# Optimization experiments

Hardware: AMD Instinct MI355X
Metric: run time of the kernel (lower is better)

The kernel has to match this reference:

```python
import jax, jax.numpy as jnp
import numpy as np

B = 262144
NUM_FEA = 256          # input feature dim, split into two towers of 128
HIDDEN = [64, 32, 16]  # tower hidden units
CO_FEA = 32            # 2 * HIDDEN[-1], features entering co-attention
EMB = 8                # per-feature embedding dim
OUT_DIM = 16           # final Dense(16)


def setup_inputs() -> dict:
    key = jax.random.key(0)
    ks = jax.random.split(key, 12)
    mid = NUM_FEA // 2
    def glorot(k, shape):
        fan_in, fan_out = shape[0], shape[1]
        lim = np.sqrt(6.0 / (fan_in + fan_out)).astype(np.float32)
        return jax.random.uniform(k, shape, jnp.float32, -lim, lim)
    return {
        "x": jax.random.normal(ks[0], (B, NUM_FEA), jnp.float32),
        # shared tower (weight_share=True -> only mod_dnn1 is used)
        "W1": glorot(ks[1], (mid, HIDDEN[0])), "b1": jnp.zeros((HIDDEN[0],), jnp.float32),
        "W2": glorot(ks[2], (HIDDEN[0], HIDDEN[1])), "b2": jnp.zeros((HIDDEN[1],), jnp.float32),
        "W3": glorot(ks[3], (HIDDEN[1], HIDDEN[2])), "b3": jnp.zeros((HIDDEN[2],), jnp.float32),
        # 32 per-feature Dense(8) layers on scalar inputs, stacked: weight [32,8], bias [32,8]
        "W_emb": glorot(ks[4], (CO_FEA, EMB)),
        "b_emb": jnp.zeros((CO_FEA, EMB), jnp.float32),
        # bilinear co-attention matrix
        "M": glorot(ks[5], (EMB, EMB)),
        # final Dense(16, relu) for mix='concat'
        "W_out": glorot(ks[6], (CO_FEA, OUT_DIM)),
        "b_out": jnp.zeros((OUT_DIM,), jnp.float32),
    }


def reference(x, W1, b1, W2, b2, W3, b3, W_emb, b_emb, M, W_out, b_out):
    mid = x.shape[1] // 2

    def tower(h):
        h = jax.nn.relu(h @ W1 + b1)
        h = jax.nn.relu(h @ W2 + b2)
        h = jax.nn.relu(h @ W3 + b3)
        return h

    left = tower(x[:, :mid])      # [B,16]
    right = tower(x[:, mid:])     # [B,16] (weight_share=True)
    out = jnp.concatenate([left, right], axis=-1)  # [B,32]

    # 32 tiny Dense(emb) on scalar features, batched: [B,32,1]*[32,8] + [32,8]
    emb = out[:, :, None] * W_emb[None, :, :] + b_emb[None, :, :]  # [B,32,8]
    cmid = out.shape[1] // 2  # 16
    l, r = emb[:, :cmid, :], emb[:, cmid:, :]

    G = jnp.tanh(jnp.einsum('bie,ef,bjf->bij', l, M, r))  # [B,16,16]
    lr = jax.nn.softmax(G.sum(axis=1), axis=-1)           # [B,16]
    rl = jax.nn.softmax(G.sum(axis=2), axis=-1)           # [B,16]
    a = jnp.concatenate([lr, rl], axis=-1)                # [B,32]

    out = out * a
    # mix == 'concat' -> Dense(16, relu)
    return jax.nn.relu(out @ W_out + b_out)               # [B,16]
```

## Files before the change

### kernel.cpp

```cpp
#include <hip/hip_runtime.h>

typedef __attribute__((ext_vector_type(8))) short bf16x8;
typedef __attribute__((ext_vector_type(4))) float f32x4;

#define MFMA16(a, b, c) __builtin_amdgcn_mfma_f32_16x16x32_bf16(a, b, c, 0, 0, 0)

__device__ __forceinline__ unsigned short f2bf(float f) {
    unsigned u = __builtin_bit_cast(unsigned, f);
    u += 0x7FFFu + ((u >> 16) & 1u);
    return (unsigned short)(u >> 16);
}
__device__ __forceinline__ float bf2f(unsigned short h) {
    return __builtin_bit_cast(float, (unsigned)h << 16);
}
__device__ __forceinline__ void split8(const float* v, bf16x8& hi, bf16x8& lo) {
    #pragma unroll
    for (int i = 0; i < 8; ++i) {
        unsigned short h = f2bf(v[i]);
        hi[i] = (short)h;
        lo[i] = (short)f2bf(v[i] - bf2f(h));
    }
}

__device__ __forceinline__ float fast_tanh(float x) {
    float e = __expf(2.0f * x);
    float r = __builtin_amdgcn_rcpf(e + 1.0f);
    return fmaf(-2.0f, r, 1.0f);
}

__global__ void prep_kernel(const float* __restrict__ W1,
                            const float* __restrict__ W2,
                            const float* __restrict__ W3,
                            const float* __restrict__ W_emb,
                            const float* __restrict__ b_emb,
                            const float* __restrict__ M,
                            float* __restrict__ pqrs,
                            unsigned short* __restrict__ w1h,
                            unsigned short* __restrict__ w1l,
                            unsigned short* __restrict__ wsm) {
    const int t = threadIdx.x;
    {
        const int j = t >> 4;
        const int i = t & 15;
        float mr[8], mb[8];
        #pragma unroll
        for (int e = 0; e < 8; ++e) {
            float ar = 0.f, ab = 0.f;
            #pragma unroll
            for (int f = 0; f < 8; ++f) {
                const float m = M[e * 8 + f];
                ar = fmaf(m, W_emb[(16 + j) * 8 + f], ar);
                ab = fmaf(m, b_emb[(16 + j) * 8 + f], ab);
            }
            mr[e] = ar; mb[e] = ab;
        }
        float P = 0.f, Q = 0.f, R = 0.f, S = 0.f;
        #pragma unroll
        for (int e = 0; e < 8; ++e) {
            const float lw = W_emb[i * 8 + e];
            const float lb = b_emb[i * 8 + e];
            P = fmaf(lw, mr[e], P);
            Q = fmaf(lw, mb[e], Q);
            R = fmaf(lb, mr[e], R);
            S = fmaf(lb, mb[e], S);
        }
        pqrs[0 * 256 + j * 16 + i] = P;
        pqrs[1 * 256 + j * 16 + i] = Q;
        pqrs[2 * 256 + j * 16 + i] = R;
        pqrs[3 * 256 + j * 16 + i] = S;
    }
    for (int e = 0; e < 32; ++e) {
        const int idx = t * 32 + e;
        const int i = idx & 7, lane = (idx >> 3) & 63;
        const int n = (idx >> 9) & 3, kt = idx >> 11;
        const int k = kt * 32 + (lane >> 4) * 8 + i;
        const int c = n * 16 + (lane & 15);
        const float v = W1[k * 64 + c];
        const unsigned short h = f2bf(v);
        w1h[idx] = h;
        w1l[idx] = f2bf(v - bf2f(h));
    }
    for (int e = 0; e < 8; ++e) {
        const int idx = t * 8 + e;
        const int i = idx & 7, lane = (idx >> 3) & 63;
        const int n = (idx >> 9) & 1, kt = (idx >> 10) & 1;
        const int k = kt * 32 + (lane >> 4) * 8 + i;
        const int c = n * 16 + (lane & 15);
        const float v = W2[k * 32 + c];
        const unsigned short h = f2bf(v);
        wsm[idx] = h;
        wsm[2048 + idx] = f2bf(v - bf2f(h));
    }
    for (int e = 0; e < 2; ++e) {
        const int idx = t * 2 + e;
        const int i = idx & 7, lane = (idx >> 3) & 63;
        const int k = (lane >> 4) * 8 + i;
        const int c = lane & 15;
        const float v = W3[k * 16 + c];
        const unsigned short h = f2bf(v);
        wsm[4096 + idx] = h;
        wsm[4608 + idx] = f2bf(v - bf2f(h));
    }
}

__global__ __launch_bounds__(256, 2) void fused_kernel(
    const float* __restrict__ x,
    const unsigned short* __restrict__ w1h,
    const unsigned short* __restrict__ w1l,
    const unsigned short* __restrict__ wsm,
    const float* __restrict__ b1, const float* __restrict__ b2,
    const float* __restrict__ b3,
    const float* __restrict__ pqrs,
    const float* __restrict__ W_out, const float* __restrict__ b_out,
    float* __restrict__ y) {
    __shared__ unsigned short s_wf[5120];
    __shared__ float s_tr[4][16 * 68];
    __shared__ float s_h3[4][64 * 20];

    const int tid = threadIdx.x;
    {
        const unsigned int* g = (const unsigned int*)wsm;
        unsigned int* s = (unsigned int*)s_wf;
        #pragma unroll
        for (int it = 0; it < 10; ++it) s[it * 256 + tid] = g[it * 256 + tid];
    }
    __syncthreads();

    const int l  = tid & 63;
    const int wv = tid >> 6;
    const int lm = l & 15;
    const int lg = l >> 4;

    const unsigned short* s_w2h = s_wf;
    const unsigned short* s_w2l = s_wf + 2048;
    const unsigned short* s_w3h = s_wf + 4096;
    const unsigned short* s_w3l = s_wf + 4608;

    float b1v[4], b2v[2];
    #pragma unroll
    for (int n = 0; n < 4; ++n) b1v[n] = b1[n * 16 + lm];
    #pragma unroll
    for (int n = 0; n < 2; ++n) b2v[n] = b2[n * 16 + lm];
    const float b3v = b3[lm];

    const long tr0 = (long)blockIdx.x * 256 + wv * 64;
    float* tb  = s_tr[wv];
    float* h3b = s_h3[wv];

    float4 xb[2][8];
    {
        const float* xp = x + (tr0 + lm) * 128 + lg * 8;
        #pragma unroll
        for (int kt = 0; kt < 4; ++kt) {
            xb[0][2 * kt]     = *(const float4*)(xp + kt * 32);
            xb[0][2 * kt + 1] = *(const float4*)(xp + kt * 32 + 4);
        }
    }

    #pragma unroll
    for (int tile = 0; tile < 4; ++tile) {
        const int cur = tile & 1, nxt = cur ^ 1;
        if (tile < 3) {
            const float* xp = x + (tr0 + (tile + 1) * 16 + lm) * 128 + lg * 8;
            #pragma unroll
            for (int kt = 0; kt < 4; ++kt) {
                xb[nxt][2 * kt]     = *(const float4*)(xp + kt * 32);
                xb[nxt][2 * kt + 1] = *(const float4*)(xp + kt * 32 + 4);
            }
        }
        f32x4 acc[4];
        #pragma unroll
        for (int n = 0; n < 4; ++n) acc[n] = f32x4{b1v[n], b1v[n], b1v[n], b1v[n]};
        #pragma unroll
        for (int kt = 0; kt < 4; ++kt) {
            const float4 a = xb[cur][2 * kt], b = xb[cur][2 * kt + 1];
            const float xv[8] = {a.x, a.y, a.z, a.w, b.x, b.y, b.z, b.w};
            bf16x8 xh, xl; split8(xv, xh, xl);
            #pragma unroll
            for (int n = 0; n < 4; ++n) {
                const int fo = ((kt * 4 + n) * 64 + l) * 8;
                const bf16x8 wh = *(const bf16x8*)(w1h + fo);
                const bf16x8 wl = *(const bf16x8*)(w1l + fo);
                acc[n] = MFMA16(xh, wh, acc[n]);
                acc[n] = MFMA16(xl, wh, acc[n]);
                acc[n] = MFMA16(xh, wl, acc[n]);
            }
        }
        #pragma unroll
        for (int n = 0; n < 4; ++n)
            #pragma unroll
            for (int r = 0; r < 4; ++r)
                tb[(lg * 4 + r) * 68 + n * 16 + lm] = fmaxf(acc[n][r], 0.f);
        f32x4 acc2[2];
        #pragma unroll
        for (int n = 0; n < 2; ++n) acc2[n] = f32x4{b2v[n], b2v[n], b2v[n], b2v[n]};
        #pragma unroll
        for (int kt = 0; kt < 2; ++kt) {
            const float* ap = tb + lm * 68 + kt * 32 + lg * 8;
            const float4 h0 = *(const float4*)(ap);
            const float4 h1 = *(const float4*)(ap + 4);
            const float hv[8] = {h0.x, h0.y, h0.z, h0.w, h1.x, h1.y, h1.z, h1.w};
            bf16x8 hh, hl; split8(hv, hh, hl);
            #pragma unroll
            for (int n = 0; n < 2; ++n) {
                const int fo = ((kt * 2 + n) * 64 + l) * 8;
                const bf16x8 wh = *(const bf16x8*)(s_w2h + fo);
                const bf16x8 wl = *(const bf16x8*)(s_w2l + fo);
                acc2[n] = MFMA16(hh, wh, acc2[n]);
                acc2[n] = MFMA16(hl, wh, acc2[n]);
                acc2[n] = MFMA16(hh, wl, acc2[n]);
            }
        }
        #pragma unroll
        for (int n = 0; n < 2; ++n)
            #pragma unroll
            for (int r = 0; r < 4; ++r)
                tb[(lg * 4 + r) * 68 + n * 16 + lm] = fmaxf(acc2[n][r], 0.f);
        f32x4 acc3 = f32x4{b3v, b3v, b3v, b3v};
        {
            const float* ap = tb + lm * 68 + lg * 8;
            const float4 h0 = *(const float4*)(ap);
            const float4 h1 = *(const float4*)(ap + 4);
            const float hv[8] = {h0.x, h0.y, h0.z, h0.w, h1.x, h1.y, h1.z, h1.w};
            bf16x8 hh, hl; split8(hv, hh, hl);
            const bf16x8 wh = *(const bf16x8*)(s_w3h + l * 8);
            const bf16x8 wl = *(const bf16x8*)(s_w3l + l * 8);
            acc3 = MFMA16(hh, wh, acc3);
            acc3 = MFMA16(hl, wh, acc3);
            acc3 = MFMA16(hh, wl, acc3);
        }
        #pragma unroll
        for (int r = 0; r < 4; ++r)
            h3b[(tile * 16 + lg * 4 + r) * 20 + lm] = fmaxf(acc3[r], 0.f);
    }

    const int p = l & 1;
    float o[16];
    {
        const float4* hp = (const float4*)(h3b + l * 20);
        const float4 t0 = hp[0], t1 = hp[1], t2 = hp[2], t3 = hp[3];
        o[0] = t0.x;  o[1] = t0.y;  o[2] = t0.z;  o[3] = t0.w;
        o[4] = t1.x;  o[5] = t1.y;  o[6] = t1.z;  o[7] = t1.w;
        o[8] = t2.x;  o[9] = t2.y;  o[10] = t2.z; o[11] = t2.w;
        o[12] = t3.x; o[13] = t3.y; o[14] = t3.z; o[15] = t3.w;
    }
    float oL[16], oR[16];
    #pragma unroll
    for (int i = 0; i < 16; ++i) {
        const float oth = __shfl_xor(o[i], 1);
        oL[i] = p ? oth : o[i];
        oR[i] = p ? o[i] : oth;
    }

    float si[16];
    #pragma unroll
    for (int i = 0; i < 16; ++i) si[i] = 0.f;
    float sj[16];
    #pragma unroll
    for (int j = 0; j < 16; ++j) {
        const float r = oR[j];
        const float* __restrict__ Pr = pqrs +       j * 16;
        const float* __restrict__ Qr = pqrs + 256 + j * 16;
        const float* __restrict__ Rr = pqrs + 512 + j * 16;
        const float* __restrict__ Sr = pqrs + 768 + j * 16;
        float accg = 0.f;
        #pragma unroll
        for (int i = 0; i < 16; ++i) {
            const float t1 = fmaf(r, Pr[i], Qr[i]);
            const float t2 = fmaf(r, Rr[i], Sr[i]);
            const float g  = fast_tanh(fmaf(oL[i], t1, t2));
            accg  += g;
            si[i] += g;
        }
        sj[j] = accg;
    }
    {
        float mx = sj[0];
        #pragma unroll
        for (int i = 1; i < 16; ++i) mx = fmaxf(mx, sj[i]);
        float s = 0.f; float ex[16];
        #pragma unroll
        for (int i = 0; i < 16; ++i) { ex[i] = __expf(sj[i] - mx); s += ex[i]; }
        const float inv = __builtin_amdgcn_rcpf(s);
        #pragma unroll
        for (int i = 0; i < 16; ++i) oL[i] *= ex[i] * inv;
    }
    {
        float mx = si[0];
        #pragma unroll
        for (int i = 1; i < 16; ++i) mx = fmaxf(mx, si[i]);
        float s = 0.f; float ex[16];
        #pragma unroll
        for (int i = 0; i < 16; ++i) { ex[i] = __expf(si[i] - mx); s += ex[i]; }
        const float inv = __builtin_amdgcn_rcpf(s);
        #pragma unroll
        for (int i = 0; i < 16; ++i) oR[i] *= ex[i] * inv;
    }

    float yv[16];
    #pragma unroll
    for (int oo = 0; oo < 16; ++oo) yv[oo] = b_out[oo];
    #pragma unroll
    for (int c = 0; c < 16; ++c) {
        const float cl = oL[c];
        const float cr = oR[c];
        const float* __restrict__ wl = W_out + c * 16;
        const float* __restrict__ wt = W_out + (16 + c) * 16;
        #pragma unroll
        for (int oo = 0; oo < 16; ++oo) {
            yv[oo] = fmaf(cl, wl[oo], yv[oo]);
            yv[oo] = fmaf(cr, wt[oo], yv[oo]);
        }
    }
    #pragma unroll
    for (int oo = 0; oo < 16; ++oo) yv[oo] = fmaxf(yv[oo], 0.f);

    float4 v0, v1;
    v0.x = p ? yv[8]  : yv[0]; v0.y = p ? yv[9]  : yv[1];
    v0.z = p ? yv[10] : yv[2]; v0.w = p ? yv[11] : yv[3];
    v1.x = p ? yv[12] : yv[4]; v1.y = p ? yv[13] : yv[5];
    v1.z = p ? yv[14] : yv[6]; v1.w = p ? yv[15] : yv[7];
    const long row = (tr0 >> 1) + (l >> 1);
    float* __restrict__ yo = y + row * 16 + p * 8;
    *reinterpret_cast<float4*>(yo)     = v0;
    *reinterpret_cast<float4*>(yo + 4) = v1;
}

extern "C" void kernel_launch(void* const* d_in, const int* in_sizes, int n_in,
                              void* d_out, int out_size, void* d_ws, size_t ws_size,
                              hipStream_t stream) {
    const float* x     = (const float*)d_in[0];
    const float* W1    = (const float*)d_in[1];
    const float* b1    = (const float*)d_in[2];
    const float* W2    = (const float*)d_in[3];
    const float* b2    = (const float*)d_in[4];
    const float* W3    = (const float*)d_in[5];
    const float* b3    = (const float*)d_in[6];
    const float* W_emb = (const float*)d_in[7];
    const float* b_emb = (const float*)d_in[8];
    const float* M     = (const float*)d_in[9];
    const float* W_out = (const float*)d_in[10];
    const float* b_out = (const float*)d_in[11];
    float* y = (float*)d_out;

    float* pqrs = (float*)d_ws;
    unsigned short* w1h = (unsigned short*)((char*)d_ws + 4096);
    unsigned short* w1l = w1h + 8192;
    unsigned short* wsm = w1l + 8192;

    const int nrows = in_sizes[0] / 256;

    prep_kernel<<<1, 256, 0, stream>>>(W1, W2, W3, W_emb, b_emb, M,
                                       pqrs, w1h, w1l, wsm);
    const int grid = nrows / 128;
    fused_kernel<<<grid, 256, 0, stream>>>(x, w1h, w1l, wsm,
                                           b1, b2, b3, pqrs, W_out, b_out, y);
}
```

Before: 152.4 us.

## Double rows per wave, drop LDS weight staging, fold tanh scaling

Each wave now processes 128 tower rows (64 output rows), so every lane owns one full output row and the shuffle-based left/right pairing goes away. W2/W3 fragments are read directly from global memory instead of being staged in LDS with a block barrier. The 2·log2(e) factor is folded into the precomputed P/Q/R/S so the inner loop uses exp2 plus rcp and applies the 1-2r affine once per row sum. The bf16 split uses packed v_cvt_pk_bf16_f32 and the launch bound asks for 3 blocks per CU. In exchange the grid is halved and global weight reads may add latency.

```diff
diff --git a/kernel.cpp b/kernel.cpp
--- a/kernel.cpp
+++ b/kernel.cpp
@@ -13,19 +13,23 @@
 __device__ __forceinline__ float bf2f(unsigned short h) {
     return __builtin_bit_cast(float, (unsigned)h << 16);
 }
+
 __device__ __forceinline__ void split8(const float* v, bf16x8& hi, bf16x8& lo) {
-    #pragma unroll
-    for (int i = 0; i < 8; ++i) {
-        unsigned short h = f2bf(v[i]);
-        hi[i] = (short)h;
-        lo[i] = (short)f2bf(v[i] - bf2f(h));
-    }
-}
-
-__device__ __forceinline__ float fast_tanh(float x) {
-    float e = __expf(2.0f * x);
-    float r = __builtin_amdgcn_rcpf(e + 1.0f);
-    return fmaf(-2.0f, r, 1.0f);
+    unsigned* hp = reinterpret_cast<unsigned*>(&hi);
+    unsigned* lp = reinterpret_cast<unsigned*>(&lo);
+    #pragma unroll
+    for (int q = 0; q < 4; ++q) {
+        const float a = v[2 * q], b = v[2 * q + 1];
+        unsigned hpair;
+        asm("v_cvt_pk_bf16_f32 %0, %1, %2" : "=v"(hpair) : "v"(a), "v"(b));
+        const float ha = __builtin_bit_cast(float, hpair << 16);
+        const float hb = __builtin_bit_cast(float, hpair & 0xFFFF0000u);
+        const float ra = a - ha, rb = b - hb;
+        unsigned lpair;
+        asm("v_cvt_pk_bf16_f32 %0, %1, %2" : "=v"(lpair) : "v"(ra), "v"(rb));
+        hp[q] = hpair;
+        lp[q] = lpair;
+    }
 }
 
 __global__ void prep_kernel(const float* __restrict__ W1,
@@ -39,6 +43,7 @@
                             unsigned short* __restrict__ w1l,
                             unsigned short* __restrict__ wsm) {
     const int t = threadIdx.x;
+    const float C2 = 2.8853900817779268f;
     {
         const int j = t >> 4;
         const int i = t & 15;
@@ -64,10 +69,10 @@
             R = fmaf(lb, mr[e], R);
             S = fmaf(lb, mb[e], S);
         }
-        pqrs[0 * 256 + j * 16 + i] = P;
-        pqrs[1 * 256 + j * 16 + i] = Q;
-        pqrs[2 * 256 + j * 16 + i] = R;
-        pqrs[3 * 256 + j * 16 + i] = S;
+        pqrs[0 * 256 + j * 16 + i] = C2 * P;
+        pqrs[1 * 256 + j * 16 + i] = C2 * Q;
+        pqrs[2 * 256 + j * 16 + i] = C2 * R;
+        pqrs[3 * 256 + j * 16 + i] = C2 * S;
     }
     for (int e = 0; e < 32; ++e) {
         const int idx = t * 32 + e;
@@ -103,7 +108,7 @@
     }
 }
 
-__global__ __launch_bounds__(256, 2) void fused_kernel(
+__global__ __launch_bounds__(256, 3) void fused_kernel(
     const float* __restrict__ x,
     const unsigned short* __restrict__ w1h,
     const unsigned short* __restrict__ w1l,
@@ -113,28 +118,19 @@
     const float* __restrict__ pqrs,
     const float* __restrict__ W_out, const float* __restrict__ b_out,
     float* __restrict__ y) {
-    __shared__ unsigned short s_wf[5120];
     __shared__ float s_tr[4][16 * 68];
-    __shared__ float s_h3[4][64 * 20];
+    __shared__ float s_h3[4][16 * 130];
 
     const int tid = threadIdx.x;
-    {
-        const unsigned int* g = (const unsigned int*)wsm;
-        unsigned int* s = (unsigned int*)s_wf;
-        #pragma unroll
-        for (int it = 0; it < 10; ++it) s[it * 256 + tid] = g[it * 256 + tid];
-    }
-    __syncthreads();
-
     const int l  = tid & 63;
     const int wv = tid >> 6;
     const int lm = l & 15;
     const int lg = l >> 4;
 
-    const unsigned short* s_w2h = s_wf;
-    const unsigned short* s_w2l = s_wf + 2048;
-    const unsigned short* s_w3h = s_wf + 4096;
-    const unsigned short* s_w3l = s_wf + 4608;
+    const unsigned short* w2h = wsm;
+    const unsigned short* w2l = wsm + 2048;
+    const unsigned short* w3h = wsm + 4096;
+    const unsigned short* w3l = wsm + 4608;
 
     float b1v[4], b2v[2];
     #pragma unroll
@@ -143,7 +139,7 @@
     for (int n = 0; n < 2; ++n) b2v[n] = b2[n * 16 + lm];
     const float b3v = b3[lm];
 
-    const long tr0 = (long)blockIdx.x * 256 + wv * 64;
+    const long tr0 = (long)blockIdx.x * 512 + wv * 128;
     float* tb  = s_tr[wv];
     float* h3b = s_h3[wv];
 
@@ -158,9 +154,9 @@
     }
 
     #pragma unroll
-    for (int tile = 0; tile < 4; ++tile) {
+    for (int tile = 0; tile < 8; ++tile) {
         const int cur = tile & 1, nxt = cur ^ 1;
-        if (tile < 3) {
+        if (tile < 7) {
             const float* xp = x + (tr0 + (tile + 1) * 16 + lm) * 128 + lg * 8;
             #pragma unroll
             for (int kt = 0; kt < 4; ++kt) {
@@ -204,8 +200,8 @@
             #pragma unroll
             for (int n = 0; n < 2; ++n) {
                 const int fo = ((kt * 2 + n) * 64 + l) * 8;
-                const bf16x8 wh = *(const bf16x8*)(s_w2h + fo);
-                const bf16x8 wl = *(const bf16x8*)(s_w2l + fo);
+                const bf16x8 wh = *(const bf16x8*)(w2h + fo);
+                const bf16x8 wl = *(const bf16x8*)(w2l + fo);
                 acc2[n] = MFMA16(hh, wh, acc2[n]);
                 acc2[n] = MFMA16(hl, wh, acc2[n]);
                 acc2[n] = MFMA16(hh, wl, acc2[n]);
@@ -223,39 +219,29 @@
             const float4 h1 = *(const float4*)(ap + 4);
             const float hv[8] = {h0.x, h0.y, h0.z, h0.w, h1.x, h1.y, h1.z, h1.w};
             bf16x8 hh, hl; split8(hv, hh, hl);
-            const bf16x8 wh = *(const bf16x8*)(s_w3h + l * 8);
-            const bf16x8 wl = *(const bf16x8*)(s_w3l + l * 8);
+            const bf16x8 wh = *(const bf16x8*)(w3h + l * 8);
+            const bf16x8 wl = *(const bf16x8*)(w3l + l * 8);
             acc3 = MFMA16(hh, wh, acc3);
             acc3 = MFMA16(hl, wh, acc3);
             acc3 = MFMA16(hh, wl, acc3);
         }
         #pragma unroll
         for (int r = 0; r < 4; ++r)
-            h3b[(tile * 16 + lg * 4 + r) * 20 + lm] = fmaxf(acc3[r], 0.f);
-    }
-
-    const int p = l & 1;
-    float o[16];
-    {
-        const float4* hp = (const float4*)(h3b + l * 20);
-        const float4 t0 = hp[0], t1 = hp[1], t2 = hp[2], t3 = hp[3];
-        o[0] = t0.x;  o[1] = t0.y;  o[2] = t0.z;  o[3] = t0.w;
-        o[4] = t1.x;  o[5] = t1.y;  o[6] = t1.z;  o[7] = t1.w;
-        o[8] = t2.x;  o[9] = t2.y;  o[10] = t2.z; o[11] = t2.w;
-        o[12] = t3.x; o[13] = t3.y; o[14] = t3.z; o[15] = t3.w;
-    }
+            h3b[lm * 130 + tile * 16 + lg * 4 + r] = fmaxf(acc3[r], 0.f);
+    }
+
     float oL[16], oR[16];
     #pragma unroll
-    for (int i = 0; i < 16; ++i) {
-        const float oth = __shfl_xor(o[i], 1);
-        oL[i] = p ? oth : o[i];
-        oR[i] = p ? o[i] : oth;
-    }
-
-    float si[16];
-    #pragma unroll
-    for (int i = 0; i < 16; ++i) si[i] = 0.f;
-    float sj[16];
+    for (int c = 0; c < 16; ++c) {
+        const float2 v = *(const float2*)(h3b + c * 130 + 2 * l);
+        oL[c] = v.x;
+        oR[c] = v.y;
+    }
+
+    float sir[16];
+    #pragma unroll
+    for (int i = 0; i < 16; ++i) sir[i] = 0.f;
+    float sjv[16];
     #pragma unroll
     for (int j = 0; j < 16; ++j) {
         const float r = oR[j];
@@ -263,35 +249,43 @@
         const float* __restrict__ Qr = pqrs + 256 + j * 16;
         const float* __restrict__ Rr = pqrs + 512 + j * 16;
         const float* __restrict__ Sr = pqrs + 768 + j * 16;
-        float accg = 0.f;
+        float accr = 0.f;
         #pragma unroll
         for (int i = 0; i < 16; ++i) {
             const float t1 = fmaf(r, Pr[i], Qr[i]);
             const float t2 = fmaf(r, Rr[i], Sr[i]);
-            const float g  = fast_tanh(fmaf(oL[i], t1, t2));
-            accg  += g;
-            si[i] += g;
-        }
-        sj[j] = accg;
-    }
+            const float z  = fmaf(oL[i], t1, t2);
+            const float e  = __builtin_amdgcn_exp2f(z);
+            const float rc = __builtin_amdgcn_rcpf(e + 1.0f);
+            accr   += rc;
+            sir[i] += rc;
+        }
+        sjv[j] = accr;
+    }
+    #pragma unroll
+    for (int i = 0; i < 16; ++i) {
+        sjv[i] = fmaf(-2.f, sjv[i], 16.f);
+        sir[i] = fmaf(-2.f, sir[i], 16.f);
+    }
+
     {
-        float mx = sj[0];
-        #pragma unroll
-        for (int i = 1; i < 16; ++i) mx = fmaxf(mx, sj[i]);
+        float mx = sjv[0];
+        #pragma unroll
+        for (int i = 1; i < 16; ++i) mx = fmaxf(mx, sjv[i]);
         float s = 0.f; float ex[16];
         #pragma unroll
-        for (int i = 0; i < 16; ++i) { ex[i] = __expf(sj[i] - mx); s += ex[i]; }
+        for (int i = 0; i < 16; ++i) { ex[i] = __expf(sjv[i] - mx); s += ex[i]; }
         const float inv = __builtin_amdgcn_rcpf(s);
         #pragma unroll
         for (int i = 0; i < 16; ++i) oL[i] *= ex[i] * inv;
     }
     {
-        float mx = si[0];
-        #pragma unroll
-        for (int i = 1; i < 16; ++i) mx = fmaxf(mx, si[i]);
+        float mx = sir[0];
+        #pragma unroll
+        for (int i = 1; i < 16; ++i) mx = fmaxf(mx, sir[i]);
         float s = 0.f; float ex[16];
         #pragma unroll
-        for (int i = 0; i < 16; ++i) { ex[i] = __expf(si[i] - mx); s += ex[i]; }
+        for (int i = 0; i < 16; ++i) { ex[i] = __expf(sir[i] - mx); s += ex[i]; }
         const float inv = __builtin_amdgcn_rcpf(s);
         #pragma unroll
         for (int i = 0; i < 16; ++i) oR[i] *= ex[i] * inv;
@@ -312,18 +306,17 @@
             yv[oo] = fmaf(cr, wt[oo], yv[oo]);
         }
     }
-    #pragma unroll
-    for (int oo = 0; oo < 16; ++oo) yv[oo] = fmaxf(yv[oo], 0.f);
-
-    float4 v0, v1;
-    v0.x = p ? yv[8]  : yv[0]; v0.y = p ? yv[9]  : yv[1];
-    v0.z = p ? yv[10] : yv[2]; v0.w = p ? yv[11] : yv[3];
-    v1.x = p ? yv[12] : yv[4]; v1.y = p ? yv[13] : yv[5];
-    v1.z = p ? yv[14] : yv[6]; v1.w = p ? yv[15] : yv[7];
-    const long row = (tr0 >> 1) + (l >> 1);
-    float* __restrict__ yo = y + row * 16 + p * 8;
-    *reinterpret_cast<float4*>(yo)     = v0;
-    *reinterpret_cast<float4*>(yo + 4) = v1;
+
+    float* __restrict__ yo = y + ((tr0 >> 1) + l) * 16;
+    #pragma unroll
+    for (int q = 0; q < 4; ++q) {
+        float4 v;
+        v.x = fmaxf(yv[q * 4 + 0], 0.f);
+        v.y = fmaxf(yv[q * 4 + 1], 0.f);
+        v.z = fmaxf(yv[q * 4 + 2], 0.f);
+        v.w = fmaxf(yv[q * 4 + 3], 0.f);
+        *reinterpret_cast<float4*>(yo + q * 4) = v;
+    }
 }
 
 extern "C" void kernel_launch(void* const* d_in, const int* in_sizes, int n_in,
@@ -352,7 +345,7 @@
 
     prep_kernel<<<1, 256, 0, stream>>>(W1, W2, W3, W_emb, b_emb, M,
                                        pqrs, w1h, w1l, wsm);
-    const int grid = nrows / 128;
+    const int grid = nrows / 256;
     fused_kernel<<<grid, 256, 0, stream>>>(x, w1h, w1l, wsm,
                                            b1, b2, b3, pqrs, W_out, b_out, y);
 }
```

After: 132.2 us. 13.3% less time.
